# Kernel tuning notes

Hardware: AMD Instinct MI355X
Metric: run time of the kernel (lower is better)

The kernel has to match this reference:

```python
import jax, jax.numpy as jnp
import numpy as np
import math

B, TQ, TK, D = 4, 1024, 1024, 1024
H, DK, DV = 16, 64, 64


def _ln(x, g, b, eps=1e-5):
    m = x.mean(-1, keepdims=True)
    v = ((x - m) ** 2).mean(-1, keepdims=True)
    return (x - m) * jax.lax.rsqrt(v + eps) * g + b


def setup_inputs() -> dict:
    key = jax.random.key(0)
    ks = jax.random.split(key, 24)
    s = 0.02
    inp = {
        "x": jax.random.normal(ks[0], (B, TQ, D), jnp.float32),
        "y": jax.random.normal(ks[1], (B, TK, D), jnp.float32),
        "mask": jax.random.randint(ks[2], (B, TK), 0, 2).astype(bool),
        # pre-attention layernorms (affine)
        "ln1_g": jnp.ones((D,)), "ln1_b": jnp.zeros((D,)),
        "ln2_g": jnp.ones((D,)), "ln2_b": jnp.zeros((D,)),
        # mha1 projections
        "q_w": jax.random.normal(ks[3], (D, H * DK)) * s, "q_b": jnp.zeros((H * DK,)),
        "k_w": jax.random.normal(ks[4], (D, H * DK)) * s, "k_b": jnp.zeros((H * DK,)),
        "v_w": jax.random.normal(ks[5], (D, H * DV)) * s, "v_b": jnp.zeros((H * DV,)),
        "o_w": jax.random.normal(ks[6], (H * DV, D)) * s, "o_b": jnp.zeros((D,)),
        # MLP: [LN, ReLU, Linear] x 2 over sizes [D, D, D]
        "mln1_g": jnp.ones((D,)), "mln1_b": jnp.zeros((D,)),
        "l1_w": jax.random.normal(ks[7], (D, D)) * s, "l1_b": jnp.zeros((D,)),
        "mln2_g": jnp.ones((D,)), "mln2_b": jnp.zeros((D,)),
        "l2_w": jax.random.normal(ks[8], (D, D)) * s, "l2_b": jnp.zeros((D,)),
    }
    return inp


def reference(x, y, mask, ln1_g, ln1_b, ln2_g, ln2_b,
              q_w, q_b, k_w, k_b, v_w, v_b, o_w, o_b,
              mln1_g, mln1_b, l1_w, l1_b, mln2_g, mln2_b, l2_w, l2_b):
    # pre-norm + relu
    x1 = jax.nn.relu(_ln(x, ln1_g, ln1_b))
    y1 = jax.nn.relu(_ln(y, ln2_g, ln2_b))
    # cross attention (mha1)
    b, t, _ = x1.shape
    q = (x1 @ q_w + q_b).reshape(b, t, H, DK)
    k = (y1 @ k_w + k_b).reshape(b, -1, H, DK)
    v = (y1 @ v_w + v_b).reshape(b, -1, H, DV)
    logits = jnp.einsum('bthd,bThd->bhtT', q, k) * (1.0 / math.sqrt(DK))
    logits = jnp.where(mask[:, None, None, :], logits, -1e30)
    w = jax.nn.softmax(logits, axis=-1)
    attn = jnp.einsum('bhtT,bThd->bthd', w, v).reshape(b, t, H * DV)
    x = x + (attn @ o_w + o_b)
    # MLP: LN -> ReLU -> Linear, twice
    h = jax.nn.relu(_ln(x, mln1_g, mln1_b)) @ l1_w + l1_b
    out = jax.nn.relu(_ln(h, mln2_g, mln2_b)) @ l2_w + l2_b
    return out
```

## Files before the change

kernel.cpp:

```cpp
#include <hip/hip_runtime.h>
#include <hip/hip_bf16.h>
#include <math.h>

#define D_MODEL 1024
#define NTOK    4096

typedef unsigned short u16;
typedef unsigned int   u32;
typedef __attribute__((ext_vector_type(8))) short  short8;
typedef __attribute__((ext_vector_type(4))) float  floatx4;
typedef __attribute__((ext_vector_type(4))) unsigned short ushort4v;
typedef __attribute__((ext_vector_type(2))) unsigned int   uint2v;

static __host__ __device__ __forceinline__ float bf2f(u16 u) {
    union { unsigned int i; float f; } v; v.i = ((unsigned int)u) << 16; return v.f;
}
static __host__ __device__ __forceinline__ u16 f2bf(float f) {
    union { float f; unsigned int i; } v; v.f = f;
    unsigned int r = (v.i + 0x7FFFu + ((v.i >> 16) & 1u)) >> 16;
    return (u16)r;
}
static __device__ __forceinline__ u32 fbits(float f) {
    union { float f; u32 i; } v; v.f = f; return v.i;
}
static __device__ __forceinline__ float fexp2(float x) {
    float r; asm("v_exp_f32 %0, %1" : "=v"(r) : "v"(x)); return r;
}
static __device__ __forceinline__ void gl2lds16(const void* g, void* l) {
    __builtin_amdgcn_global_load_lds(
        (const __attribute__((address_space(1))) void*)g,
        (__attribute__((address_space(3))) void*)l, 16, 0, 0);
}

__global__ __launch_bounds__(256) void CrossTransformer_27522150432886_kernel(
    float* __restrict__ out, int n, float val)
{
    int i = blockIdx.x * 256 + threadIdx.x;
    if (i < n) out[i] = val;
}

struct PreArgs {
    const float* w[6]; u16* wt;
    const float* x; const float* g1; const float* b1; u16* xn;
    const float* y; const float* g2; const float* b2; u16* yn;
    const void* maskp; float* madd;
};
__global__ __launch_bounds__(256) void pre_k(PreArgs a)
{
    __shared__ __align__(16) char shm[2176];
    const int blk = blockIdx.x, t = threadIdx.x;

    if (blk < 6144) {
        u16 (*tile)[33] = (u16(*)[33])shm;
        const int wz = blk >> 10, tl = blk & 1023;
        const int c0 = (tl & 31) * 32, r0 = (tl >> 5) * 32;
        const int tx = t & 31, ty = t >> 5;
        const float* W  = a.w[wz];
        u16*         Wt = a.wt + (size_t)wz * D_MODEL * D_MODEL;
#pragma unroll
        for (int j = 0; j < 4; j++)
            tile[ty + j * 8][tx] = f2bf(W[(size_t)(r0 + ty + j * 8) * D_MODEL + c0 + tx]);
        __syncthreads();
#pragma unroll
        for (int j = 0; j < 4; j++)
            Wt[(size_t)(c0 + ty + j * 8) * D_MODEL + r0 + tx] = tile[tx][ty + j * 8];
        return;
    }
    if (blk < 14336) {
        const int isY = blk >= 10240;
        const int row = blk - (isY ? 10240 : 6144);
        const float* in  = isY ? a.y  : a.x;
        const float* gam = isY ? a.g2 : a.g1;
        const float* bet = isY ? a.b2 : a.b1;
        u16*         out = isY ? a.yn : a.xn;
        float (*red)[4] = (float(*)[4])shm;

        const float4 p = *(const float4*)(in + (size_t)row * D_MODEL + t * 4);
        float v0 = p.x, v1 = p.y, v2 = p.z, v3 = p.w;
        float s = v0 + v1 + v2 + v3;
        float q = v0 * v0 + v1 * v1 + v2 * v2 + v3 * v3;
#pragma unroll
        for (int off = 32; off > 0; off >>= 1) {
            s += __shfl_xor(s, off, 64);
            q += __shfl_xor(q, off, 64);
        }
        if ((t & 63) == 0) { red[0][t >> 6] = s; red[1][t >> 6] = q; }
        __syncthreads();
        s = red[0][0] + red[0][1] + red[0][2] + red[0][3];
        q = red[1][0] + red[1][1] + red[1][2] + red[1][3];
        const float mean = s * (1.0f / D_MODEL);
        const float var  = q * (1.0f / D_MODEL) - mean * mean;
        const float rstd = rsqrtf(var + 1e-5f);
        const float4 gp = *(const float4*)(gam + t * 4);
        const float4 bp = *(const float4*)(bet + t * 4);
        ushort4v o;
        o[0] = f2bf(fmaxf((v0 - mean) * rstd * gp.x + bp.x, 0.f));
        o[1] = f2bf(fmaxf((v1 - mean) * rstd * gp.y + bp.y, 0.f));
        o[2] = f2bf(fmaxf((v2 - mean) * rstd * gp.z + bp.z, 0.f));
        o[3] = f2bf(fmaxf((v3 - mean) * rstd * gp.w + bp.w, 0.f));
        *(ushort4v*)(out + (size_t)row * D_MODEL + t * 4) = o;
        return;
    }
    {
        int* rb = (int*)shm;
        const unsigned int* wv = (const unsigned int*)a.maskp;
        int bad = 0;
        for (int i = t; i < 1024; i += 256) {
            unsigned int v = wv[i];
            if (!(v == 0u || v == 1u || v == 0xFFu || v == 0xFFFFFFFFu)) bad++;
        }
#pragma unroll
        for (int off = 32; off > 0; off >>= 1) bad += __shfl_xor(bad, off, 64);
        if ((t & 63) == 0) rb[t >> 6] = bad;
        __syncthreads();
        const int Bc = rb[0] + rb[1] + rb[2] + rb[3];
        if (Bc * 2 > 1024) {
            const unsigned char* b8 = (const unsigned char*)a.maskp;
            for (int i = t; i < 4096; i += 256) a.madd[i] = b8[i] ? 0.f : -1e30f;
        } else {
            const int* m32 = (const int*)a.maskp;
            for (int i = t; i < 4096; i += 256) a.madd[i] = m32[i] ? 0.f : -1e30f;
        }
    }
}

__global__ __launch_bounds__(256) void ln_relu_k(
    const void* __restrict__ in, const float* __restrict__ gam,
    const float* __restrict__ bet, u16* __restrict__ out)
{
    const int row = blockIdx.x, t = threadIdx.x;
    ushort4v u = *(const ushort4v*)((const u16*)in + (size_t)row * D_MODEL + t * 4);
    float v0 = bf2f(u[0]), v1 = bf2f(u[1]), v2 = bf2f(u[2]), v3 = bf2f(u[3]);
    float s = v0 + v1 + v2 + v3;
    float q = v0 * v0 + v1 * v1 + v2 * v2 + v3 * v3;
#pragma unroll
    for (int off = 32; off > 0; off >>= 1) {
        s += __shfl_xor(s, off, 64);
        q += __shfl_xor(q, off, 64);
    }
    __shared__ float red[2][4];
    if ((t & 63) == 0) { red[0][t >> 6] = s; red[1][t >> 6] = q; }
    __syncthreads();
    s = red[0][0] + red[0][1] + red[0][2] + red[0][3];
    q = red[1][0] + red[1][1] + red[1][2] + red[1][3];

    const float mean = s * (1.0f / D_MODEL);
    const float var  = q * (1.0f / D_MODEL) - mean * mean;
    const float rstd = rsqrtf(var + 1e-5f);

    const float4 gp = *(const float4*)(gam + t * 4);
    const float4 bp = *(const float4*)(bet + t * 4);
    ushort4v o;
    o[0] = f2bf(fmaxf((v0 - mean) * rstd * gp.x + bp.x, 0.f));
    o[1] = f2bf(fmaxf((v1 - mean) * rstd * gp.y + bp.y, 0.f));
    o[2] = f2bf(fmaxf((v2 - mean) * rstd * gp.z + bp.z, 0.f));
    o[3] = f2bf(fmaxf((v3 - mean) * rstd * gp.w + bp.w, 0.f));
    *(ushort4v*)(out + (size_t)row * D_MODEL + t * 4) = o;
}

struct GB {
    const u16* A; const u16* Bt; const float* bias; const float* resid;
    u16* C; float* Cf; float scale; int vt;
};
struct GB3 { GB g[3]; u16* VtG; };

template<int NS>
__global__ __launch_bounds__(256) void gemm128_k(GB3 gb, int cpx)
{
    const int lin = blockIdx.x + 8 * blockIdx.y + 256 * blockIdx.z;
    const int t8  = (lin & 7) * cpx + (lin >> 3);
    const int z   = t8 >> 8;
    const int rem = t8 & 255;
    const GB cfg = gb.g[z];
    __shared__ __align__(16) u16 sm[NS * 8192];
    const int t = threadIdx.x, lane = t & 63, w = t >> 6;
    const int wy = w >> 1, wx = w & 1;
    const int bm = (rem >> 3) * 128, bn = (rem & 7) * 128;
    const int m = lane & 15, g = lane >> 4;
    const int arow = t >> 2;
    const int aseg = ((t & 3) ^ ((t >> 3) & 3)) * 8;
    const int gsw  = (g ^ ((m >> 1) & 3)) * 8;

    const u16* Ag = cfg.A  + (size_t)(bm + arow) * D_MODEL + aseg;
    const u16* Bg = cfg.Bt + (size_t)(bn + arow) * D_MODEL + aseg;

    auto stage = [&](int k0, int s) {
        char* dst = (char*)sm + s * 16384;
#pragma unroll
        for (int i = 0; i < 2; i++) {
            gl2lds16(Ag + (size_t)(i * 64) * D_MODEL + k0, dst + i * 4096 + w * 1024);
            gl2lds16(Bg + (size_t)(i * 64) * D_MODEL + k0, dst + 8192 + i * 4096 + w * 1024);
        }
    };

    floatx4 acc[4][4] = {};
    const int NT = D_MODEL / 32;

#pragma unroll
    for (int i = 0; i < NS - 1; i++) stage(i * 32, i);
    if constexpr (NS == 3) asm volatile("s_waitcnt vmcnt(4)" ::: "memory");
    else                   asm volatile("s_waitcnt vmcnt(8)" ::: "memory");
    __builtin_amdgcn_s_barrier();

    int sb = 0;
    for (int tt = 0; tt < NT; ++tt) {
        int tp = tt + (NS - 1); if (tp >= NT) tp -= NT;
        int sbp = sb + (NS - 1); if (sbp >= NS) sbp -= NS;
        stage(tp * 32, sbp);

        const u16* As = sm + sb * 8192;
        const u16* Bs = As + 4096;
        short8 af[4], bf[4];
#pragma unroll
        for (int mt = 0; mt < 4; mt++)
            af[mt] = *(const short8*)(As + (wy * 64 + mt * 16 + m) * 32 + gsw);
#pragma unroll
        for (int nt = 0; nt < 4; nt++)
            bf[nt] = *(const short8*)(Bs + (wx * 64 + nt * 16 + m) * 32 + gsw);

        __builtin_amdgcn_s_setprio(1);
#pragma unroll
        for (int mt = 0; mt < 4; mt++)
#pragma unroll
            for (int nt = 0; nt < 4; nt++)
                acc[mt][nt] = __builtin_amdgcn_mfma_f32_16x16x32_bf16(
                    af[mt], bf[nt], acc[mt][nt], 0, 0, 0);
        __builtin_amdgcn_s_setprio(0);

        if constexpr (NS == 3) asm volatile("s_waitcnt vmcnt(4)" ::: "memory");
        else                   asm volatile("s_waitcnt vmcnt(8)" ::: "memory");
        __builtin_amdgcn_s_barrier();
        sb = sb + 1; if (sb >= NS) sb -= NS;
    }
    asm volatile("s_waitcnt vmcnt(0)" ::: "memory");
    __builtin_amdgcn_s_barrier();

    float bv[4];
#pragma unroll
    for (int nt = 0; nt < 4; nt++)
        bv[nt] = cfg.bias[bn + wx * 64 + nt * 16 + m];

    if (!cfg.vt) {
#pragma unroll
        for (int mt = 0; mt < 4; mt++)
#pragma unroll
            for (int r = 0; r < 4; r++) {
                const int grow = bm + wy * 64 + mt * 16 + g * 4 + r;
#pragma unroll
                for (int nt = 0; nt < 4; nt++) {
                    const int col = bn + wx * 64 + nt * 16 + m;
                    float val = (acc[mt][nt][r] + bv[nt]) * cfg.scale;
                    if (cfg.resid) val += cfg.resid[(size_t)grow * D_MODEL + col];
                    if (cfg.Cf) cfg.Cf[(size_t)grow * D_MODEL + col] = val;
                    else        cfg.C [(size_t)grow * D_MODEL + col] = f2bf(val);
                }
            }
    } else {
        u16* Lt = sm;
        const int b16  = (bm >> 10) * 16;
        const int bn6  = bn >> 6;
        const int tok0 = bm & 1023;
#pragma unroll
        for (int hh = 0; hh < 2; hh++) {
            if (wx == hh) {
#pragma unroll
                for (int mt = 0; mt < 4; mt++)
#pragma unroll
                    for (int r = 0; r < 4; r++) {
                        const int tok = wy * 64 + mt * 16 + g * 4 + r;
#pragma unroll
                        for (int nt = 0; nt < 4; nt++) {
                            const int d = nt * 16 + m;
                            Lt[d * 128 + (((tok >> 3) ^ (d & 15)) << 3) + (tok & 7)] =
                                f2bf(acc[mt][nt][r] + bv[nt]);
                        }
                    }
            }
            __syncthreads();
#pragma unroll
            for (int j = 0; j < 4; j++) {
                const int s = j * 256 + t;
                const int d = s >> 4, c = s & 15;
                short8 v = *(const short8*)(Lt + d * 128 + ((c ^ (d & 15)) << 3));
                *(short8*)(gb.VtG + ((size_t)((b16 + bn6 + hh) * 64 + d)) * 1024 + tok0 + c * 8) = v;
            }
            __syncthreads();
        }
    }
}

__global__ __launch_bounds__(256) void attn_k(
    const u16* __restrict__ Q, const u16* __restrict__ Kk,
    const u16* __restrict__ VtG, const float* __restrict__ maddG,
    u16* __restrict__ Ob)
{
    __shared__ __align__(16) char smraw[55808];
    u16*   KsB  = (u16*)smraw;
    u16*   VtB  = (u16*)(smraw + 16384);
    u16*   Ps   = (u16*)(smraw + 32768);
    float* madd = (float*)(smraw + 51200);
    float* liS  = (float*)(smraw + 55296);

    const int lin = blockIdx.x + 8 * (blockIdx.y + 16 * blockIdx.z);
    const int tw  = (lin & 7) * 64 + (lin >> 3);
    const int qt = tw & 7, h = (tw >> 3) & 15, b = tw >> 7;
    const int t = threadIdx.x, lane = t & 63, w = t >> 6;
    const int m = lane & 15, g = lane >> 4;

    for (int i = t; i < 1024; i += 256) madd[i] = maddG[b * 1024 + i];

    short8 qf[2][2];
    const u16* Qb = Q + ((size_t)(b * 1024 + qt * 128 + w * 32 + m)) * D_MODEL + h * 64 + g * 8;
#pragma unroll
    for (int q2 = 0; q2 < 2; q2++)
#pragma unroll
        for (int hf = 0; hf < 2; hf++)
            qf[q2][hf] = *(const short8*)(Qb + q2 * 16 * D_MODEL + hf * 32);

    u16* Pw = Ps + w * 32 * 72;
    const u16* Kp = Kk  + (size_t)(b * 1024) * D_MODEL + h * 64;
    const u16* Vp = VtG + (size_t)((b * 16 + h) * 64) * 1024;

    const int r0 = lane >> 3;
    const int ssl = ((lane & 7) ^ r0) * 8;
    auto stageKV = [&](int kt, int bufI) {
#pragma unroll
        for (int i = 0; i < 2; i++) {
            const int row = w * 16 + i * 8 + r0;
            gl2lds16(Kp + (size_t)(kt + row) * D_MODEL + ssl,
                     (char*)(KsB + bufI * 4096) + (w * 2 + i) * 1024);
            gl2lds16(Vp + (size_t)row * 1024 + kt + ssl,
                     (char*)(VtB + bufI * 4096) + (w * 2 + i) * 1024);
        }
    };

    floatx4 Ov[2][4] = {};
    float li[2] = { 0.f, 0.f };

    const int s8  = m & 7;
    const int sl0 = (g ^ s8) * 8;
    const int sl1 = sl0 ^ 32;

    stageKV(0, 0);
    __syncthreads();

    int buf = 0;
    for (int kt = 0; kt < 1024; kt += 64) {
        if (kt + 64 < 1024) stageKV(kt + 64, buf ^ 1);

        const u16* Ks = KsB + buf * 4096;
        const u16* Vt = VtB + buf * 4096;

        short8 af[4][2];
        float4 md[4];
#pragma unroll
        for (int tile = 0; tile < 4; tile++) {
            af[tile][0] = *(const short8*)(Ks + (tile * 16 + m) * 64 + sl0);
            af[tile][1] = *(const short8*)(Ks + (tile * 16 + m) * 64 + sl1);
            md[tile]    = *(const float4*)(madd + kt + tile * 16 + g * 4);
        }

#pragma unroll
        for (int q2 = 0; q2 < 2; q2++) {
            floatx4 st[4];
            __builtin_amdgcn_s_setprio(1);
#pragma unroll
            for (int tile = 0; tile < 4; tile++) {
                floatx4 z = {};
                z = __builtin_amdgcn_mfma_f32_16x16x32_bf16(af[tile][0], qf[q2][0], z, 0, 0, 0);
                st[tile] = __builtin_amdgcn_mfma_f32_16x16x32_bf16(af[tile][1], qf[q2][1], z, 0, 0, 0);
            }
            __builtin_amdgcn_s_setprio(0);
            float rs = 0.f;
#pragma unroll
            for (int tile = 0; tile < 4; tile++) {
                float p0 = fexp2(st[tile][0] + md[tile].x);
                float p1 = fexp2(st[tile][1] + md[tile].y);
                float p2 = fexp2(st[tile][2] + md[tile].z);
                float p3 = fexp2(st[tile][3] + md[tile].w);
                rs += (p0 + p1) + (p2 + p3);
                uint2v pk;
                pk[0] = __builtin_amdgcn_perm(fbits(p1), fbits(p0), 0x07060302u);
                pk[1] = __builtin_amdgcn_perm(fbits(p3), fbits(p2), 0x07060302u);
                *(uint2v*)(Pw + (q2 * 16 + m) * 72 + tile * 16 + g * 4) = pk;
            }
            rs += __shfl_xor(rs, 16, 64);
            rs += __shfl_xor(rs, 32, 64);
            li[q2] += rs;
        }

        short8 pa[2][2], vb[4][2];
#pragma unroll
        for (int q2 = 0; q2 < 2; q2++) {
            pa[q2][0] = *(const short8*)(Pw + (q2 * 16 + m) * 72 + g * 8);
            pa[q2][1] = *(const short8*)(Pw + (q2 * 16 + m) * 72 + 32 + g * 8);
        }
#pragma unroll
        for (int nt = 0; nt < 4; nt++) {
            vb[nt][0] = *(const short8*)(Vt + (nt * 16 + m) * 64 + sl0);
            vb[nt][1] = *(const short8*)(Vt + (nt * 16 + m) * 64 + sl1);
        }
        __builtin_amdgcn_s_setprio(1);
#pragma unroll
        for (int q2 = 0; q2 < 2; q2++)
#pragma unroll
            for (int nt = 0; nt < 4; nt++) {
                Ov[q2][nt] = __builtin_amdgcn_mfma_f32_16x16x32_bf16(
                    pa[q2][0], vb[nt][0], Ov[q2][nt], 0, 0, 0);
                Ov[q2][nt] = __builtin_amdgcn_mfma_f32_16x16x32_bf16(
                    pa[q2][1], vb[nt][1], Ov[q2][nt], 0, 0, 0);
            }
        __builtin_amdgcn_s_setprio(0);

        asm volatile("s_waitcnt vmcnt(0)" ::: "memory");
        __builtin_amdgcn_s_barrier();
        buf ^= 1;
    }

    if (g == 0) { liS[w * 32 + m] = li[0]; liS[w * 32 + 16 + m] = li[1]; }
    __builtin_amdgcn_s_waitcnt(0);
    float4 inv4[2];
#pragma unroll
    for (int q2 = 0; q2 < 2; q2++) {
        float4 l4 = *(const float4*)(liS + w * 32 + q2 * 16 + g * 4);
        inv4[q2].x = 1.0f / fmaxf(l4.x, 1e-37f);
        inv4[q2].y = 1.0f / fmaxf(l4.y, 1e-37f);
        inv4[q2].z = 1.0f / fmaxf(l4.z, 1e-37f);
        inv4[q2].w = 1.0f / fmaxf(l4.w, 1e-37f);
    }
#pragma unroll
    for (int q2 = 0; q2 < 2; q2++) {
        const float iv[4] = { inv4[q2].x, inv4[q2].y, inv4[q2].z, inv4[q2].w };
#pragma unroll
        for (int nt = 0; nt < 4; nt++)
#pragma unroll
            for (int r = 0; r < 4; r++) {
                const int tok = qt * 128 + w * 32 + q2 * 16 + g * 4 + r;
                Ob[(size_t)(b * 1024 + tok) * D_MODEL + h * 64 + nt * 16 + m] =
                    f2bf(Ov[q2][nt][r] * iv[r]);
            }
    }
}

extern "C" __attribute__((visibility("default")))
void kernel_launch(void* const* d_in, const int* in_sizes, int n_in,
                   void* d_out, int out_size, void* d_ws, size_t ws_size,
                   hipStream_t stream)
{
    (void)in_sizes; (void)n_in;
    const float* x      = (const float*)d_in[0];
    const float* y      = (const float*)d_in[1];
    const void*  maskp  = d_in[2];
    const float* ln1_g  = (const float*)d_in[3];
    const float* ln1_b  = (const float*)d_in[4];
    const float* ln2_g  = (const float*)d_in[5];
    const float* ln2_b  = (const float*)d_in[6];
    const float* q_w    = (const float*)d_in[7];
    const float* q_b    = (const float*)d_in[8];
    const float* k_w    = (const float*)d_in[9];
    const float* k_b    = (const float*)d_in[10];
    const float* v_w    = (const float*)d_in[11];
    const float* v_b    = (const float*)d_in[12];
    const float* o_w    = (const float*)d_in[13];
    const float* o_b    = (const float*)d_in[14];
    const float* mln1_g = (const float*)d_in[15];
    const float* mln1_b = (const float*)d_in[16];
    const float* l1_w   = (const float*)d_in[17];
    const float* l1_b   = (const float*)d_in[18];
    const float* mln2_g = (const float*)d_in[19];
    const float* mln2_b = (const float*)d_in[20];
    const float* l2_w   = (const float*)d_in[21];
    const float* l2_b   = (const float*)d_in[22];

    const int nout = out_size;
    const size_t MB = 1024 * 1024;
    if (ws_size < 61 * MB) {
        CrossTransformer_27522150432886_kernel<<<(nout + 255) / 256, 256, 0, stream>>>(
            (float*)d_out, nout, 7.0f);
        return;
    }

    char* ws = (char*)d_ws;
    const size_t WE = (size_t)D_MODEL * D_MODEL;
    u16*   wt   = (u16*)(ws);
    u16*   xn   = (u16*)(ws + 12 * MB);
    u16*   yn   = (u16*)(ws + 20 * MB);
    u16*   Qb   = (u16*)(ws + 28 * MB);
    u16*   Kb   = (u16*)(ws + 36 * MB);
    u16*   VtG  = (u16*)(ws + 44 * MB);
    u16*   attn = (u16*)(ws + 52 * MB);
    float* madd = (float*)(ws + 60 * MB);
    u16* x2 = xn; u16* m1n = Qb; u16* hb = Kb; u16* m2n = VtG;

    PreArgs pa;
    pa.w[0] = q_w; pa.w[1] = k_w; pa.w[2] = v_w;
    pa.w[3] = o_w; pa.w[4] = l1_w; pa.w[5] = l2_w;
    pa.wt = wt;
    pa.x = x; pa.g1 = ln1_g; pa.b1 = ln1_b; pa.xn = xn;
    pa.y = y; pa.g2 = ln2_g; pa.b2 = ln2_b; pa.yn = yn;
    pa.maskp = maskp; pa.madd = madd;
    pre_k<<<14337, 256, 0, stream>>>(pa);

    const float qscale = 0.18033688011112042f;
    GB3 qkv = {};
    qkv.g[0] = GB{ xn, wt + 0 * WE, q_b, nullptr, Qb, nullptr, qscale, 0 };
    qkv.g[1] = GB{ yn, wt + 1 * WE, k_b, nullptr, Kb, nullptr, 1.0f,  0 };
    qkv.g[2] = GB{ yn, wt + 2 * WE, v_b, nullptr, nullptr, nullptr, 1.0f, 1 };
    qkv.VtG = VtG;
    gemm128_k<3><<<dim3(8, 32, 3), 256, 0, stream>>>(qkv, 96);

    attn_k<<<dim3(8, 16, 4), 256, 0, stream>>>(Qb, Kb, VtG, madd, attn);

    GB3 go = {};
    go.g[0] = GB{ attn, wt + 3 * WE, o_b, x, x2, nullptr, 1.0f, 0 };
    gemm128_k<4><<<dim3(8, 32, 1), 256, 0, stream>>>(go, 32);

    ln_relu_k<<<NTOK, 256, 0, stream>>>(x2, mln1_g, mln1_b, m1n);

    GB3 g1 = {};
    g1.g[0] = GB{ m1n, wt + 4 * WE, l1_b, nullptr, hb, nullptr, 1.0f, 0 };
    gemm128_k<4><<<dim3(8, 32, 1), 256, 0, stream>>>(g1, 32);

    ln_relu_k<<<NTOK, 256, 0, stream>>>(hb, mln2_g, mln2_b, m2n);

    GB3 g2 = {};
    g2.g[0] = GB{ m2n, wt + 5 * WE, l2_b, nullptr, nullptr, (float*)d_out, 1.0f, 0 };
    gemm128_k<4><<<dim3(8, 32, 1), 256, 0, stream>>>(g2, 32);
}
```

Before: 296.0 us.

## Use 512-thread 8-wave GEMM with 3-stage pipeline for single-projection GEMMs

The templated GEMM is split into a dedicated QKV kernel and a new single-output kernel for the out-projection and both MLP linears. The new kernel runs 8 waves per 128x128 tile, each wave computing 64x32, with a 3-stage LDS pipeline instead of 4. Only 256 blocks exist for these GEMMs on a chip with many CUs, so more waves per block aims to improve latency hiding and per-CU throughput. The trade-off is fewer accumulators per wave (lower MFMA-to-LDS-read ratio) and a shallower prefetch.

```diff
diff --git a/kernel.cpp b/kernel.cpp
--- a/kernel.cpp
+++ b/kernel.cpp
@@ -164,15 +164,14 @@
 };
 struct GB3 { GB g[3]; u16* VtG; };
 
-template<int NS>
-__global__ __launch_bounds__(256) void gemm128_k(GB3 gb, int cpx)
+__global__ __launch_bounds__(256) void gemm_qkv_k(GB3 gb)
 {
     const int lin = blockIdx.x + 8 * blockIdx.y + 256 * blockIdx.z;
-    const int t8  = (lin & 7) * cpx + (lin >> 3);
+    const int t8  = (lin & 7) * 96 + (lin >> 3);
     const int z   = t8 >> 8;
     const int rem = t8 & 255;
     const GB cfg = gb.g[z];
-    __shared__ __align__(16) u16 sm[NS * 8192];
+    __shared__ __align__(16) u16 sm[3 * 8192];
     const int t = threadIdx.x, lane = t & 63, w = t >> 6;
     const int wy = w >> 1, wx = w & 1;
     const int bm = (rem >> 3) * 128, bn = (rem & 7) * 128;
@@ -196,16 +195,15 @@
     floatx4 acc[4][4] = {};
     const int NT = D_MODEL / 32;
 
-#pragma unroll
-    for (int i = 0; i < NS - 1; i++) stage(i * 32, i);
-    if constexpr (NS == 3) asm volatile("s_waitcnt vmcnt(4)" ::: "memory");
-    else                   asm volatile("s_waitcnt vmcnt(8)" ::: "memory");
+    stage(0, 0);
+    stage(32, 1);
+    asm volatile("s_waitcnt vmcnt(4)" ::: "memory");
     __builtin_amdgcn_s_barrier();
 
     int sb = 0;
     for (int tt = 0; tt < NT; ++tt) {
-        int tp = tt + (NS - 1); if (tp >= NT) tp -= NT;
-        int sbp = sb + (NS - 1); if (sbp >= NS) sbp -= NS;
+        int tp = tt + 2; if (tp >= NT) tp -= NT;
+        int sbp = sb + 2; if (sbp >= 3) sbp -= 3;
         stage(tp * 32, sbp);
 
         const u16* As = sm + sb * 8192;
@@ -227,10 +225,9 @@
                     af[mt], bf[nt], acc[mt][nt], 0, 0, 0);
         __builtin_amdgcn_s_setprio(0);
 
-        if constexpr (NS == 3) asm volatile("s_waitcnt vmcnt(4)" ::: "memory");
-        else                   asm volatile("s_waitcnt vmcnt(8)" ::: "memory");
+        asm volatile("s_waitcnt vmcnt(4)" ::: "memory");
         __builtin_amdgcn_s_barrier();
-        sb = sb + 1; if (sb >= NS) sb -= NS;
+        sb = sb + 1; if (sb >= 3) sb -= 3;
     }
     asm volatile("s_waitcnt vmcnt(0)" ::: "memory");
     __builtin_amdgcn_s_barrier();
@@ -250,9 +247,7 @@
                 for (int nt = 0; nt < 4; nt++) {
                     const int col = bn + wx * 64 + nt * 16 + m;
                     float val = (acc[mt][nt][r] + bv[nt]) * cfg.scale;
-                    if (cfg.resid) val += cfg.resid[(size_t)grow * D_MODEL + col];
-                    if (cfg.Cf) cfg.Cf[(size_t)grow * D_MODEL + col] = val;
-                    else        cfg.C [(size_t)grow * D_MODEL + col] = f2bf(val);
+                    cfg.C[(size_t)grow * D_MODEL + col] = f2bf(val);
                 }
             }
     } else {
@@ -285,6 +280,89 @@
                 *(short8*)(gb.VtG + ((size_t)((b16 + bn6 + hh) * 64 + d)) * 1024 + tok0 + c * 8) = v;
             }
             __syncthreads();
+        }
+    }
+}
+
+__global__ __launch_bounds__(512) void gemm_out_k(GB cfg)
+{
+    const int lin = blockIdx.x + 8 * blockIdx.y;
+    const int t8  = (lin & 7) * 32 + (lin >> 3);
+    __shared__ __align__(16) u16 sm[3 * 8192];
+    const int t = threadIdx.x, lane = t & 63, w = t >> 6;
+    const int wy = w >> 2, wx = w & 3;
+    const int bm = (t8 >> 3) * 128, bn = (t8 & 7) * 128;
+    const int m = lane & 15, g = lane >> 4;
+    const int arow = t >> 2;
+    const int aseg = ((t & 3) ^ ((t >> 3) & 3)) * 8;
+    const int gsw  = (g ^ ((m >> 1) & 3)) * 8;
+
+    const u16* Ag = cfg.A  + (size_t)(bm + arow) * D_MODEL + aseg;
+    const u16* Bg = cfg.Bt + (size_t)(bn + arow) * D_MODEL + aseg;
+
+    auto stage = [&](int k0, int s) {
+        char* dst = (char*)sm + s * 16384;
+        gl2lds16(Ag + k0, dst + w * 1024);
+        gl2lds16(Bg + k0, dst + 8192 + w * 1024);
+    };
+
+    floatx4 acc[4][2] = {};
+    const int NT = D_MODEL / 32;
+
+    stage(0, 0);
+    stage(32, 1);
+    asm volatile("s_waitcnt vmcnt(2)" ::: "memory");
+    __builtin_amdgcn_s_barrier();
+
+    int sb = 0;
+    for (int tt = 0; tt < NT; ++tt) {
+        int tp = tt + 2; if (tp >= NT) tp -= NT;
+        int sbp = sb + 2; if (sbp >= 3) sbp -= 3;
+        stage(tp * 32, sbp);
+
+        const u16* As = sm + sb * 8192;
+        const u16* Bs = As + 4096;
+        short8 af[4], bf[2];
+#pragma unroll
+        for (int mt = 0; mt < 4; mt++)
+            af[mt] = *(const short8*)(As + (wy * 64 + mt * 16 + m) * 32 + gsw);
+#pragma unroll
+        for (int nt = 0; nt < 2; nt++)
+            bf[nt] = *(const short8*)(Bs + (wx * 32 + nt * 16 + m) * 32 + gsw);
+
+        __builtin_amdgcn_s_setprio(1);
+#pragma unroll
+        for (int mt = 0; mt < 4; mt++)
+#pragma unroll
+            for (int nt = 0; nt < 2; nt++)
+                acc[mt][nt] = __builtin_amdgcn_mfma_f32_16x16x32_bf16(
+                    af[mt], bf[nt], acc[mt][nt], 0, 0, 0);
+        __builtin_amdgcn_s_setprio(0);
+
+        asm volatile("s_waitcnt vmcnt(2)" ::: "memory");
+        __builtin_amdgcn_s_barrier();
+        sb = sb + 1; if (sb >= 3) sb -= 3;
+    }
+    asm volatile("s_waitcnt vmcnt(0)" ::: "memory");
+
+    float bv[2]; int cols[2];
+#pragma unroll
+    for (int nt = 0; nt < 2; nt++) {
+        cols[nt] = bn + wx * 32 + nt * 16 + m;
+        bv[nt]   = cfg.bias[cols[nt]];
+    }
+#pragma unroll
+    for (int mt = 0; mt < 4; mt++) {
+#pragma unroll
+        for (int r = 0; r < 4; r++) {
+            const int grow = bm + wy * 64 + mt * 16 + g * 4 + r;
+#pragma unroll
+            for (int nt = 0; nt < 2; nt++) {
+                float val = acc[mt][nt][r] + bv[nt];
+                if (cfg.resid) val += cfg.resid[(size_t)grow * D_MODEL + cols[nt]];
+                if (cfg.Cf) cfg.Cf[(size_t)grow * D_MODEL + cols[nt]] = val;
+                else        cfg.C [(size_t)grow * D_MODEL + cols[nt]] = f2bf(val);
+            }
         }
     }
 }
@@ -507,23 +585,20 @@
     qkv.g[1] = GB{ yn, wt + 1 * WE, k_b, nullptr, Kb, nullptr, 1.0f,  0 };
     qkv.g[2] = GB{ yn, wt + 2 * WE, v_b, nullptr, nullptr, nullptr, 1.0f, 1 };
     qkv.VtG = VtG;
-    gemm128_k<3><<<dim3(8, 32, 3), 256, 0, stream>>>(qkv, 96);
+    gemm_qkv_k<<<dim3(8, 32, 3), 256, 0, stream>>>(qkv);
 
     attn_k<<<dim3(8, 16, 4), 256, 0, stream>>>(Qb, Kb, VtG, madd, attn);
 
-    GB3 go = {};
-    go.g[0] = GB{ attn, wt + 3 * WE, o_b, x, x2, nullptr, 1.0f, 0 };
-    gemm128_k<4><<<dim3(8, 32, 1), 256, 0, stream>>>(go, 32);
+    GB go = GB{ attn, wt + 3 * WE, o_b, x, x2, nullptr, 1.0f, 0 };
+    gemm_out_k<<<dim3(8, 32, 1), 512, 0, stream>>>(go);
 
     ln_relu_k<<<NTOK, 256, 0, stream>>>(x2, mln1_g, mln1_b, m1n);
 
-    GB3 g1 = {};
-    g1.g[0] = GB{ m1n, wt + 4 * WE, l1_b, nullptr, hb, nullptr, 1.0f, 0 };
-    gemm128_k<4><<<dim3(8, 32, 1), 256, 0, stream>>>(g1, 32);
+    GB g1 = GB{ m1n, wt + 4 * WE, l1_b, nullptr, hb, nullptr, 1.0f, 0 };
+    gemm_out_k<<<dim3(8, 32, 1), 512, 0, stream>>>(g1);
 
     ln_relu_k<<<NTOK, 256, 0, stream>>>(hb, mln2_g, mln2_b, m2n);
 
-    GB3 g2 = {};
-    g2.g[0] = GB{ m2n, wt + 5 * WE, l2_b, nullptr, nullptr, (float*)d_out, 1.0f, 0 };
-    gemm128_k<4><<<dim3(8, 32, 1), 256, 0, stream>>>(g2, 32);
-}
+    GB g2 = GB{ m2n, wt + 5 * WE, l2_b, nullptr, nullptr, (float*)d_out, 1.0f, 0 };
+    gemm_out_k<<<dim3(8, 32, 1), 512, 0, stream>>>(g2);
+}
```

After: 278.8 us. 5.8% less time.
